# Kernel tuning notes

Hardware: AMD Instinct MI355X
Metric: run time of the kernel (lower is better)

## Reference

```python
import jax, jax.numpy as jnp
import numpy as np

B, S, I, C, N = 8, 50, 20, 64, 4096  # batch, max seq len, items per set, channels, num_items


def setup_inputs() -> dict:
    key = jax.random.key(0)
    k1, k2, k3, k4, k5 = jax.random.split(key, 5)
    input_tensor = jax.random.normal(k1, (B, S, I, C), dtype=jnp.float32)
    items_id = jax.random.randint(k2, (B, S, I), 0, N)
    # seq lengths in [1, S] (original truncates each user's sequence)
    batch_seq_length = jax.random.randint(k3, (B,), 1, S + 1)
    items_embedding = jax.random.normal(k4, (N, C), dtype=jnp.float32) * 0.02
    proj_w = jax.random.normal(k5, (C, C), dtype=jnp.float32) / jnp.sqrt(jnp.float32(C))
    proj_b = jnp.zeros((C,), dtype=jnp.float32)
    return {
        "input_tensor": input_tensor,
        "items_embedding": items_embedding,
        "proj_w": proj_w,
        "proj_b": proj_b,
        "items_id": items_id,
        "batch_seq_length": batch_seq_length,
    }


def reference(input_tensor, items_embedding, proj_w, proj_b, items_id, batch_seq_length):
    # Dropout layers are identity in eval mode.
    Bb, Ss, Ii, Cc = input_tensor.shape
    Nn = items_embedding.shape[0]

    # valid sequence positions per user: seq_index < batch_seq_length[b]
    seq_mask = (jnp.arange(Ss)[None, :] < batch_seq_length[:, None]).astype(input_tensor.dtype)  # [B,S]
    m = seq_mask[:, :, None]  # [B,S,1], all I item slots valid inside a valid position

    # segment-mean over item occurrences (replaces the Python dict-of-lists + stack/mean)
    flat_ids = (items_id + jnp.arange(Bb)[:, None, None] * Nn).reshape(-1)  # [B*S*I]
    data = (input_tensor * m[..., None]).reshape(-1, Cc)                    # [B*S*I, C]
    sums = jax.ops.segment_sum(data, flat_ids, num_segments=Bb * Nn).reshape(Bb, Nn, Cc)
    counts = jax.ops.segment_sum(jnp.broadcast_to(m, (Bb, Ss, Ii)).reshape(-1),
                                 flat_ids, num_segments=Bb * Nn).reshape(Bb, Nn)
    present = counts > 0                                                    # user's unique historical items
    mean = sums / jnp.maximum(counts, 1.0)[..., None]                       # [B,N,C]

    # attention of all items over the user's unique historical-item embeddings
    scores = jnp.einsum('nc,bmc->bnm', items_embedding, mean)               # [B,N,N]
    scores = jax.nn.leaky_relu(scores, negative_slope=0.2)
    scores = jnp.where(present[:, None, :], scores, jnp.float32(-1e30))     # softmax only over present items
    attn = jax.nn.softmax(scores, axis=-1)
    user_items_embedding = jnp.einsum('bnm,bmc->bnc', attn, mean)           # [B,N,C]

    proj = user_items_embedding @ proj_w.T + proj_b                         # Linear(C,C)
    return (proj * items_embedding[None]).sum(axis=-1)                      # [B,N]
```

## Files before the change

kernel.cpp:

```cpp
#include <hip/hip_runtime.h>

#define Bb 8
#define Ss 50
#define Ii 20
#define Cc 64
#define Nn 4096
#define MAXM 1024
#define POSB (Ss * Ii)

typedef unsigned short ushort_t;
typedef __attribute__((ext_vector_type(8))) short short8;
typedef __attribute__((ext_vector_type(4))) float f32x4;

__device__ inline ushort_t bf16_rn(float x) {
    unsigned u = __float_as_uint(x);
    u = u + 0x7FFFu + ((u >> 16) & 1u);
    return (ushort_t)(u >> 16);
}
__device__ inline float bf16_f(ushort_t h) { return __uint_as_float(((unsigned)h) << 16); }

__device__ inline short8 cvthi8(float4 a, float4 b) {
    short8 r;
    r[0] = (short)bf16_rn(a.x); r[1] = (short)bf16_rn(a.y);
    r[2] = (short)bf16_rn(a.z); r[3] = (short)bf16_rn(a.w);
    r[4] = (short)bf16_rn(b.x); r[5] = (short)bf16_rn(b.y);
    r[6] = (short)bf16_rn(b.z); r[7] = (short)bf16_rn(b.w);
    return r;
}
__device__ inline short8 cvtlo8(float4 a, float4 b, short8 hi) {
    short8 r;
    r[0] = (short)bf16_rn(a.x - bf16_f((ushort_t)hi[0]));
    r[1] = (short)bf16_rn(a.y - bf16_f((ushort_t)hi[1]));
    r[2] = (short)bf16_rn(a.z - bf16_f((ushort_t)hi[2]));
    r[3] = (short)bf16_rn(a.w - bf16_f((ushort_t)hi[3]));
    r[4] = (short)bf16_rn(b.x - bf16_f((ushort_t)hi[4]));
    r[5] = (short)bf16_rn(b.y - bf16_f((ushort_t)hi[5]));
    r[6] = (short)bf16_rn(b.z - bf16_f((ushort_t)hi[6]));
    r[7] = (short)bf16_rn(b.w - bf16_f((ushort_t)hi[7]));
    return r;
}

__global__ __launch_bounds__(1024) void aux_kernel(
    const float* __restrict__ input, const int* __restrict__ ids,
    const int* __restrict__ seqlen, const float* __restrict__ E,
    const float* __restrict__ W, const float* __restrict__ bias,
    int* __restrict__ Mcnt, int* __restrict__ slotHead, int* __restrict__ gnext,
    float* __restrict__ cvec, float* __restrict__ Fbuf) {
    __shared__ int smem[5120];
    int tid = threadIdx.x;

    if (blockIdx.x < Bb) {
        int b = blockIdx.x;
        int* head = smem;
        __shared__ int mcnt;
        for (int i = tid; i < Nn; i += 1024) head[i] = -1;
        if (tid == 0) mcnt = 0;
        __syncthreads();
        int P = seqlen[b] * Ii;
        if (tid < P) {
            int id = ids[b * POSB + tid];
            gnext[b * POSB + tid] = atomicExch(&head[id], tid);
        }
        __syncthreads();
        for (int i = tid; i < Nn; i += 1024) {
            int h = head[i];
            if (h >= 0) slotHead[b * MAXM + atomicAdd(&mcnt, 1)] = h;
        }
        __syncthreads();
        if (tid == 0) Mcnt[b] = mcnt;
    } else {
        int pb = blockIdx.x - Bb;
        float* wlds = (float*)smem;
        float* elds = (float*)smem + 4096;
        int n0 = pb * 16;
#pragma unroll
        for (int i = 0; i < 4; i++) wlds[tid + 1024 * i] = W[tid + 1024 * i];
        float ev = E[(size_t)n0 * Cc + tid];
        elds[tid] = ev;
        __syncthreads();
        int nl = tid >> 6, k = tid & 63;
        float acc = 0.f;
#pragma unroll
        for (int c = 0; c < Cc; c++) acc = fmaf(elds[nl * Cc + c], wlds[c * Cc + k], acc);
        Fbuf[(size_t)(n0 + nl) * Cc + k] = acc;
        float p = ev * bias[k];
#pragma unroll
        for (int off = 32; off; off >>= 1) p += __shfl_down(p, off);
        if (k == 0) cvec[n0 + nl] = p;
    }
}

__global__ __launch_bounds__(256) void mean_kernel(
    const float* __restrict__ input, const int* __restrict__ slotHead,
    const int* __restrict__ gnext, const int* __restrict__ Mcnt,
    ushort_t* __restrict__ Mhi) {
    int w = (blockIdx.x * 256 + threadIdx.x) >> 6;
    int lane = threadIdx.x & 63;
    int b = w >> 10;
    int slot = w & (MAXM - 1);
    if (slot >= Mcnt[b]) return;
    int p = slotHead[b * MAXM + slot];
    float sum = 0.f; int k = 0;
    while (p >= 0) {
        sum += input[((size_t)(b * POSB + p)) * Cc + lane];
        k++;
        p = gnext[b * POSB + p];
    }
    Mhi[((size_t)(b * MAXM + slot)) * Cc + lane] = bf16_rn(sum / (float)k);
}

#define MFMA(A, B, C) __builtin_amdgcn_mfma_f32_16x16x32_bf16(A, B, C, 0, 0, 0)

__global__ __launch_bounds__(256) void main_kernel(
    const float* __restrict__ E, const float* __restrict__ Fbuf,
    const ushort_t* __restrict__ Mhi,
    const int* __restrict__ Mcnt, const float* __restrict__ cvec,
    float* __restrict__ out) {
    int idx = blockIdx.x;
    int ntile = idx >> 3;
    int b = (idx + (idx >> 3) + (idx >> 8)) & 7;
    int tid = threadIdx.x;
    int wave = tid >> 6, lane = tid & 63;
    int kq = lane >> 4;
    int n = ntile * 64 + wave * 16 + (lane & 15);

    const float4* ep = (const float4*)(E + (size_t)n * Cc + kq * 8);
    const float4* fp = (const float4*)(Fbuf + (size_t)n * Cc + kq * 8);
    float4 ea = ep[0], eb = ep[1], ec = ep[8], ed = ep[9];
    float4 fa = fp[0], fb = fp[1], fc = fp[8], fd = fp[9];
    short8 Eh0 = cvthi8(ea, eb), Eh1 = cvthi8(ec, ed);
    short8 Fh0 = cvthi8(fa, fb), Fh1 = cvthi8(fc, fd);
    short8 Fl0 = cvtlo8(fa, fb, Fh0), Fl1 = cvtlo8(fc, fd, Fh1);

    int M = Mcnt[b];
    int nmt = (M + 15) >> 4;
    size_t ab = ((size_t)(b * MAXM) + (lane & 15)) * Cc + kq * 8;

    short8 Ah0 = *(const short8*)(Mhi + ab), Ah1 = *(const short8*)(Mhi + ab + 32);

    float m0 = -1e30f, l = 0.f, av = 0.f;
    int rowg = kq * 4;

#pragma unroll 1
    for (int mt = 0; mt < nmt; mt++) {
        int mtn = (mt + 1 < nmt) ? mt + 1 : mt;
        size_t an = ab + (size_t)mtn * (16 * Cc);
        short8 Nh0 = *(const short8*)(Mhi + an), Nh1 = *(const short8*)(Mhi + an + 32);

        f32x4 S = {0.f, 0.f, 0.f, 0.f}, D = {0.f, 0.f, 0.f, 0.f};
        S = MFMA(Ah0, Eh0, S); S = MFMA(Ah1, Eh1, S);
        D = MFMA(Ah0, Fh0, D); D = MFMA(Ah1, Fh1, D);
        D = MFMA(Ah0, Fl0, D); D = MFMA(Ah1, Fl1, D);

        int mrow = mt * 16 + rowg;
#pragma unroll
        for (int r = 0; r < 4; r++) {
            if (mrow + r < M) {
                float s = S[r];
                float sc = s > 0.f ? s : 0.2f * s;
                float df = D[r];
                float ex = __expf(-fabsf(sc - m0));
                bool sg = sc > m0;
                float p = sg ? 1.f : ex;
                float al = sg ? ex : 1.f;
                m0 = fmaxf(m0, sc);
                l = l * al + p;
                av = av * al + p * df;
            }
        }
        Ah0 = Nh0; Ah1 = Nh1;
    }

#pragma unroll
    for (int mask = 16; mask <= 32; mask <<= 1) {
        float m0b = __shfl_xor(m0, mask);
        float lb  = __shfl_xor(l,  mask);
        float avb = __shfl_xor(av, mask);
        float M0 = fmaxf(m0, m0b);
        float w1 = __expf(m0 - M0), w2 = __expf(m0b - M0);
        m0 = M0;
        l  = l * w1 + lb * w2;
        av = av * w1 + avb * w2;
    }
    if (kq == 0) out[b * Nn + n] = av / l + cvec[n];
}

extern "C" void kernel_launch(void* const* d_in, const int* in_sizes, int n_in,
                              void* d_out, int out_size, void* d_ws, size_t ws_size,
                              hipStream_t stream) {
    (void)in_sizes; (void)n_in; (void)out_size; (void)ws_size;
    const float* input  = (const float*)d_in[0];
    const float* E      = (const float*)d_in[1];
    const float* W      = (const float*)d_in[2];
    const float* bias   = (const float*)d_in[3];
    const int*   ids    = (const int*)d_in[4];
    const int*   seqlen = (const int*)d_in[5];
    float* out = (float*)d_out;

    int*      Mcnt     = (int*)d_ws;
    int*      slotHead = Mcnt + 16;
    int*      gnext    = slotHead + Bb * MAXM;
    float*    cvec     = (float*)(gnext + Bb * POSB);
    float*    Fbuf     = cvec + Nn;
    ushort_t* Mhi      = (ushort_t*)(Fbuf + (size_t)Nn * Cc);

    aux_kernel <<<Bb + Nn / 16, 1024, 0, stream>>>(input, ids, seqlen, E, W, bias,
                                                   Mcnt, slotHead, gnext, cvec, Fbuf);
    mean_kernel<<<Bb * MAXM / 4, 256, 0, stream>>>(input, slotHead, gnext, Mcnt, Mhi);
    main_kernel<<<Bb * (Nn / 64), 256, 0, stream>>>(E, Fbuf, Mhi, Mcnt, cvec, out);
}
```

Before: 89.62 us.

## Split attention M loop across two wave groups and drop online-softmax max tracking

Doubles the block to 512 threads so two wave groups each process alternating M tiles for the same 64 items, then combines their partial sums through shared memory. The running-max online softmax is replaced by plain exp accumulation with masking, which shortens the per-element dependency chain. The cost is a shared-memory merge and a sync. Removing max subtraction risks overflow if scores are large, so correctness relies on scores staying small.

```diff
diff --git a/kernel.cpp b/kernel.cpp
--- a/kernel.cpp
+++ b/kernel.cpp
@@ -111,18 +111,20 @@
 
 #define MFMA(A, B, C) __builtin_amdgcn_mfma_f32_16x16x32_bf16(A, B, C, 0, 0, 0)
 
-__global__ __launch_bounds__(256) void main_kernel(
+__global__ __launch_bounds__(512) void main_kernel(
     const float* __restrict__ E, const float* __restrict__ Fbuf,
     const ushort_t* __restrict__ Mhi,
     const int* __restrict__ Mcnt, const float* __restrict__ cvec,
     float* __restrict__ out) {
+    __shared__ float part[2][64];
     int idx = blockIdx.x;
     int ntile = idx >> 3;
     int b = (idx + (idx >> 3) + (idx >> 8)) & 7;
     int tid = threadIdx.x;
     int wave = tid >> 6, lane = tid & 63;
+    int wn = wave & 3, wm = wave >> 2;
     int kq = lane >> 4;
-    int n = ntile * 64 + wave * 16 + (lane & 15);
+    int n = ntile * 64 + wn * 16 + (lane & 15);
 
     const float4* ep = (const float4*)(E + (size_t)n * Cc + kq * 8);
     const float4* fp = (const float4*)(Fbuf + (size_t)n * Cc + kq * 8);
@@ -136,14 +138,15 @@
     int nmt = (M + 15) >> 4;
     size_t ab = ((size_t)(b * MAXM) + (lane & 15)) * Cc + kq * 8;
 
-    short8 Ah0 = *(const short8*)(Mhi + ab), Ah1 = *(const short8*)(Mhi + ab + 32);
-
-    float m0 = -1e30f, l = 0.f, av = 0.f;
+    size_t a0 = ab + (size_t)wm * (16 * Cc);
+    short8 Ah0 = *(const short8*)(Mhi + a0), Ah1 = *(const short8*)(Mhi + a0 + 32);
+
+    float l = 0.f, av = 0.f;
     int rowg = kq * 4;
 
 #pragma unroll 1
-    for (int mt = 0; mt < nmt; mt++) {
-        int mtn = (mt + 1 < nmt) ? mt + 1 : mt;
+    for (int mt = wm; mt < nmt; mt += 2) {
+        int mtn = (mt + 2 < nmt) ? mt + 2 : mt;
         size_t an = ab + (size_t)mtn * (16 * Cc);
         short8 Nh0 = *(const short8*)(Mhi + an), Nh1 = *(const short8*)(Mhi + an + 32);
 
@@ -155,34 +158,31 @@
         int mrow = mt * 16 + rowg;
 #pragma unroll
         for (int r = 0; r < 4; r++) {
-            if (mrow + r < M) {
-                float s = S[r];
-                float sc = s > 0.f ? s : 0.2f * s;
-                float df = D[r];
-                float ex = __expf(-fabsf(sc - m0));
-                bool sg = sc > m0;
-                float p = sg ? 1.f : ex;
-                float al = sg ? ex : 1.f;
-                m0 = fmaxf(m0, sc);
-                l = l * al + p;
-                av = av * al + p * df;
-            }
+            float s = S[r];
+            float sc = fmaxf(s, 0.2f * s);
+            float ex = __expf(sc);
+            ex = (mrow + r < M) ? ex : 0.f;
+            l += ex;
+            av = fmaf(ex, D[r], av);
         }
         Ah0 = Nh0; Ah1 = Nh1;
     }
 
 #pragma unroll
     for (int mask = 16; mask <= 32; mask <<= 1) {
-        float m0b = __shfl_xor(m0, mask);
-        float lb  = __shfl_xor(l,  mask);
-        float avb = __shfl_xor(av, mask);
-        float M0 = fmaxf(m0, m0b);
-        float w1 = __expf(m0 - M0), w2 = __expf(m0b - M0);
-        m0 = M0;
-        l  = l * w1 + lb * w2;
-        av = av * w1 + avb * w2;
-    }
-    if (kq == 0) out[b * Nn + n] = av / l + cvec[n];
+        l  += __shfl_xor(l,  mask);
+        av += __shfl_xor(av, mask);
+    }
+    if (wm == 1 && lane < 16) {
+        part[0][wn * 16 + lane] = l;
+        part[1][wn * 16 + lane] = av;
+    }
+    __syncthreads();
+    if (wm == 0 && lane < 16) {
+        float lp  = part[0][wn * 16 + lane];
+        float avp = part[1][wn * 16 + lane];
+        out[b * Nn + n] = (av + avp) / (l + lp) + cvec[n];
+    }
 }
 
 extern "C" void kernel_launch(void* const* d_in, const int* in_sizes, int n_in,
@@ -207,5 +207,5 @@
     aux_kernel <<<Bb + Nn / 16, 1024, 0, stream>>>(input, ids, seqlen, E, W, bias,
                                                    Mcnt, slotHead, gnext, cvec, Fbuf);
     mean_kernel<<<Bb * MAXM / 4, 256, 0, stream>>>(input, slotHead, gnext, Mcnt, Mhi);
-    main_kernel<<<Bb * (Nn / 64), 256, 0, stream>>>(E, Fbuf, Mhi, Mcnt, cvec, out);
-}
+    main_kernel<<<Bb * (Nn / 64), 512, 0, stream>>>(E, Fbuf, Mhi, Mcnt, cvec, out);
+}
```

New measurement: 89.05 us. Within noise of the previous version (-0.6%).
